# Performance work log

Hardware: AMD Instinct MI355X
Metric: run time of the kernel (lower is better)

The kernel has to match this reference:

```python
import jax, jax.numpy as jnp
import numpy as np

B, S, A, C, E, H = 256, 512, 8, 256, 64, 256

def _lin_params(key, din, dout):
    k1, k2 = jax.random.split(key)
    bound = 1.0 / np.sqrt(din)
    w = jax.random.uniform(k1, (din, dout), minval=-bound, maxval=bound, dtype=jnp.float32)
    b = jax.random.uniform(k2, (dout,), minval=-bound, maxval=bound, dtype=jnp.float32)
    return w, b

def setup_inputs() -> dict:
    key = jax.random.key(0)
    ks = jax.random.split(key, 9)
    q = jax.random.normal(ks[0], (B, S, A), dtype=jnp.float32)
    st = jax.random.normal(ks[1], (B, S, C), dtype=jnp.float32)
    w1a, b1a = _lin_params(ks[2], C, H)
    w1b, b1b = _lin_params(ks[3], H, A * E)
    w2a, b2a = _lin_params(ks[4], C, H)
    w2b, b2b = _lin_params(ks[5], H, E)
    wb1, bb1 = _lin_params(ks[6], C, E)
    wb2a, bb2a = _lin_params(ks[7], C, H)
    wb2b, bb2b = _lin_params(ks[8], H, 1)
    return dict(agent_q_values=q, central_states=st,
                w1a=w1a, b1a=b1a, w1b=w1b, b1b=b1b,
                w2a=w2a, b2a=b2a, w2b=w2b, b2b=b2b,
                wb1=wb1, bb1=bb1,
                wb2a=wb2a, bb2a=bb2a, wb2b=wb2b, bb2b=bb2b)

def _mlp(x, wa, ba, wb, bb):
    # Linear -> ELU -> Linear
    h = jax.nn.elu(x @ wa + ba)
    return h @ wb + bb

def reference(agent_q_values, central_states,
              w1a, b1a, w1b, b1b,
              w2a, b2a, w2b, b2b,
              wb1, bb1,
              wb2a, bb2a, wb2b, bb2b):
    bsz, seq, na = agent_q_values.shape
    st = central_states.reshape(-1, C)                      # [N, C]
    q = agent_q_values.reshape(-1, na)                      # [N, A]
    w1 = jnp.abs(_mlp(st, w1a, b1a, w1b, b1b)).reshape(-1, na, E)   # [N, A, E]
    b1 = st @ wb1 + bb1                                     # [N, E]
    w2 = jnp.abs(_mlp(st, w2a, b2a, w2b, b2b))              # [N, E]
    b2 = _mlp(st, wb2a, bb2a, wb2b, bb2b)                   # [N, 1]
    hidden = jax.nn.relu(jnp.einsum('na,nae->ne', q, w1) + b1)      # [N, E]
    joint = jnp.einsum('ne,ne->n', hidden, w2)[:, None] + b2        # [N, 1]
    return joint.reshape(bsz, seq, 1)
```

## Files before the change

kernel.cpp:

```cpp
#include <hip/hip_runtime.h>
#include <math.h>

typedef __bf16 bf16_t;
typedef bf16_t bf16x8 __attribute__((ext_vector_type(8)));
typedef float  floatx4 __attribute__((ext_vector_type(4)));

#define MFMA16(a, b, c) __builtin_amdgcn_mfma_f32_16x16x32_bf16((a), (b), (c), 0, 0, 0)

constexpr int NTOT = 256 * 512;
constexpr int CDIM = 256;

constexpr int N_TILES  = 88;
constexpr int WS_ELEMS = N_TILES * 4096;

__global__ void prep_weights(const float* __restrict__ w1a, const float* __restrict__ w1b,
                             const float* __restrict__ w2a, const float* __restrict__ w2b,
                             const float* __restrict__ wb1, const float* __restrict__ wb2a,
                             bf16_t* __restrict__ ws) {
  int idx = blockIdx.x * 256 + threadIdx.x;
  if (idx >= WS_ELEMS) return;
  int t   = idx >> 12;
  int rel = idx & 4095;
  const float* src; int dout; int ct;
  if      (t < 16) { src = w1a;  dout = 256; ct = t; }
  else if (t < 20) { src = wb1;  dout = 64;  ct = t - 16; }
  else if (t < 52) { src = w1b;  dout = 512; ct = t - 20; }
  else if (t < 68) { src = w2a;  dout = 256; ct = t - 52; }
  else if (t < 72) { src = w2b;  dout = 64;  ct = t - 68; }
  else             { src = wb2a; dout = 256; ct = t - 72; }
  int j    = rel & 7;
  int lane = (rel >> 3) & 63;
  int ks   = rel >> 9;
  int o = ct * 16 + (lane & 15);
  int k = ks * 32 + (lane >> 4) * 8 + j;
  ws[idx] = (bf16_t)src[(size_t)k * dout + o];
}

__device__ __forceinline__ void gload_lds16(const bf16_t* g, bf16_t* l) {
  __builtin_amdgcn_global_load_lds(
      (const __attribute__((address_space(1))) unsigned int*)g,
      (__attribute__((address_space(3))) unsigned int*)l, 16, 0, 0);
}

__global__ __launch_bounds__(256, 4)
void mixing_fused(const float* __restrict__ q,
                  const float* __restrict__ st,
                  const bf16_t* __restrict__ W,
                  const float* __restrict__ b1a, const float* __restrict__ b1b,
                  const float* __restrict__ b2a, const float* __restrict__ b2b,
                  const float* __restrict__ bb1,
                  const float* __restrict__ bb2a,
                  const float* __restrict__ wb2b, const float* __restrict__ bb2b,
                  float* __restrict__ out) {
  __shared__ __align__(16) bf16_t wbuf[2][8192];
  __shared__ __align__(16) bf16_t t_s[4][16][36];
  __shared__ __align__(16) float  q_s[4][128];

  const int tid  = threadIdx.x;
  const int wid  = tid >> 6;
  const int lane = tid & 63;
  const int l15  = lane & 15;
  const int quad = lane >> 4;
  const int m0   = blockIdx.x * 64 + wid * 16;

  auto stage = [&](int g) {
    const bf16_t* src = W + (size_t)g * 8192 + wid * 2048 + lane * 8;
    bf16_t* dst = &wbuf[g & 1][wid * 2048];
#pragma unroll
    for (int i = 0; i < 4; ++i)
      gload_lds16(src + i * 512, dst + i * 512);
  };

  *(float2*)&q_s[wid][lane * 2] = *(const float2*)(q + (size_t)m0 * 8 + lane * 2);

  bf16x8 sA[8];
  {
    const float* rp = st + (size_t)(m0 + l15) * CDIM;
#pragma unroll
    for (int ks = 0; ks < 8; ++ks) {
      int k0 = ks * 32 + quad * 8;
      float4 f0 = *(const float4*)(rp + k0);
      float4 f1 = *(const float4*)(rp + k0 + 4);
      bf16x8 v;
      v[0] = (bf16_t)f0.x; v[1] = (bf16_t)f0.y; v[2] = (bf16_t)f0.z; v[3] = (bf16_t)f0.w;
      v[4] = (bf16_t)f1.x; v[5] = (bf16_t)f1.y; v[6] = (bf16_t)f1.z; v[7] = (bf16_t)f1.w;
      sA[ks] = v;
    }
  }

  auto gemmL = [&](int buf, int h, const bf16x8 (&A)[8], floatx4& acc) {
    floatx4 z = {0.f, 0.f, 0.f, 0.f};
    acc = z;
#pragma unroll
    for (int kk = 0; kk < 8; ++kk) {
      bf16x8 b = *(const bf16x8*)&wbuf[buf][h * 4096 + kk * 512 + lane * 8];
      acc = MFMA16(A[kk], b, acc);
    }
  };

  stage(0);

  bf16x8 hA[8];

#pragma unroll
  for (int ks = 0; ks < 8; ++ks) {
    __syncthreads();
    stage(ks + 1);
    const int buf = ks & 1;
#pragma unroll
    for (int h = 0; h < 2; ++h) {
      int ct = 2 * ks + h;
      floatx4 acc;
      gemmL(buf, h, sA, acc);
      float bias = b1a[ct * 16 + l15];
#pragma unroll
      for (int i = 0; i < 4; ++i) {
        float v = acc[i] + bias;
        v = v > 0.f ? v : (__expf(v) - 1.f);
        t_s[wid][quad * 4 + i][h * 16 + l15] = (bf16_t)v;
      }
    }
    hA[ks] = *(const bf16x8*)&t_s[wid][l15][quad * 8];
  }

  floatx4 hid[4];
#pragma unroll
  for (int gg = 0; gg < 2; ++gg) {
    __syncthreads();
    stage(9 + gg);
    const int buf = gg & 1;
#pragma unroll
    for (int h = 0; h < 2; ++h) {
      int et = 2 * gg + h;
      floatx4 acc;
      gemmL(buf, h, sA, acc);
      float bias = bb1[et * 16 + l15];
      hid[et] = acc + bias;
    }
  }

#pragma unroll 1
  for (int a = 0; a < 8; ++a) {
    float qv[4];
#pragma unroll
    for (int i = 0; i < 4; ++i)
      qv[i] = q_s[wid][(quad * 4 + i) * 8 + a];
#pragma unroll
    for (int g2 = 0; g2 < 2; ++g2) {
      const int idx = a * 2 + g2;
      __syncthreads();
      stage(11 + idx);
      const int buf = g2;
#pragma unroll
      for (int h = 0; h < 2; ++h) {
        int ct = a * 4 + g2 * 2 + h;
        const int et = g2 * 2 + h;
        floatx4 acc;
        gemmL(buf, h, hA, acc);
        float bias = b1b[ct * 16 + l15];
#pragma unroll
        for (int i = 0; i < 4; ++i) {
          float w1v = fabsf(acc[i] + bias);
          hid[et][i] += qv[i] * w1v;
        }
      }
    }
  }
#pragma unroll
  for (int et = 0; et < 4; ++et)
#pragma unroll
    for (int i = 0; i < 4; ++i) hid[et][i] = fmaxf(hid[et][i], 0.f);

#pragma unroll
  for (int ks = 0; ks < 8; ++ks) {
    __syncthreads();
    stage(27 + ks);
    const int buf = ks & 1;
#pragma unroll
    for (int h = 0; h < 2; ++h) {
      int ct = 2 * ks + h;
      floatx4 acc;
      gemmL(buf, h, sA, acc);
      float bias = b2a[ct * 16 + l15];
#pragma unroll
      for (int i = 0; i < 4; ++i) {
        float v = acc[i] + bias;
        v = v > 0.f ? v : (__expf(v) - 1.f);
        t_s[wid][quad * 4 + i][h * 16 + l15] = (bf16_t)v;
      }
    }
    hA[ks] = *(const bf16x8*)&t_s[wid][l15][quad * 8];
  }

  float p[4] = {0.f, 0.f, 0.f, 0.f};
#pragma unroll
  for (int gg = 0; gg < 2; ++gg) {
    __syncthreads();
    stage(35 + gg);
    const int buf = gg & 1;
#pragma unroll
    for (int h = 0; h < 2; ++h) {
      int et = 2 * gg + h;
      floatx4 acc;
      gemmL(buf, h, hA, acc);
      float bias = b2b[et * 16 + l15];
#pragma unroll
      for (int i = 0; i < 4; ++i) {
        float w2v = fabsf(acc[i] + bias);
        p[i] += hid[et][i] * w2v;
      }
    }
  }

#pragma unroll 1
  for (int gg = 0; gg < 8; ++gg) {
    __syncthreads();
    if (gg < 7) stage(37 + gg);
    const int buf = gg & 1;
#pragma unroll
    for (int h = 0; h < 2; ++h) {
      int ct = 2 * gg + h;
      floatx4 acc;
      gemmL(buf, h, sA, acc);
      float bias = bb2a[ct * 16 + l15];
      float wv   = wb2b[ct * 16 + l15];
#pragma unroll
      for (int i = 0; i < 4; ++i) {
        float v = acc[i] + bias;
        v = v > 0.f ? v : (__expf(v) - 1.f);
        p[i] += v * wv;
      }
    }
  }

  float bb2 = bb2b[0];
#pragma unroll
  for (int i = 0; i < 4; ++i) {
    float v = p[i];
    v += __shfl_xor(v, 1);
    v += __shfl_xor(v, 2);
    v += __shfl_xor(v, 4);
    v += __shfl_xor(v, 8);
    if (l15 == 0) out[m0 + quad * 4 + i] = v + bb2;
  }
}

extern "C" void kernel_launch(void* const* d_in, const int* in_sizes, int n_in,
                              void* d_out, int out_size, void* d_ws, size_t ws_size,
                              hipStream_t stream) {
  const float* q    = (const float*)d_in[0];
  const float* st   = (const float*)d_in[1];
  const float* w1a  = (const float*)d_in[2];
  const float* b1a  = (const float*)d_in[3];
  const float* w1b  = (const float*)d_in[4];
  const float* b1b  = (const float*)d_in[5];
  const float* w2a  = (const float*)d_in[6];
  const float* b2a  = (const float*)d_in[7];
  const float* w2b  = (const float*)d_in[8];
  const float* b2b  = (const float*)d_in[9];
  const float* wb1  = (const float*)d_in[10];
  const float* bb1  = (const float*)d_in[11];
  const float* wb2a = (const float*)d_in[12];
  const float* bb2a = (const float*)d_in[13];
  const float* wb2b = (const float*)d_in[14];
  const float* bb2b = (const float*)d_in[15];
  bf16_t* W = (bf16_t*)d_ws;

  hipLaunchKernelGGL(prep_weights, dim3((WS_ELEMS + 255) / 256), dim3(256), 0, stream,
                     w1a, w1b, w2a, w2b, wb1, wb2a, W);
  hipLaunchKernelGGL(mixing_fused, dim3(NTOT / 64), dim3(256), 0, stream,
                     q, st, W, b1a, b1b, b2a, b2b, bb1, bb2a, wb2b, bb2b, (float*)d_out);
}
```

Baseline: 320.3 us.

## Split weight tiles between LDS staging and direct global-to-register loads

Each 8192-element weight group is now split in half: the first 4096-element column tile is still staged into LDS via global_load_lds, and the second tile is loaded straight from global memory into registers (Bd) for its MFMA sequence. This halves LDS usage and the LDS read traffic per group. The cost is higher register pressure, so launch bounds drop from 4 to 3 blocks per CU, and the direct global loads may sit on the critical path with latency that is not hidden.

```diff
diff --git a/kernel.cpp b/kernel.cpp
--- a/kernel.cpp
+++ b/kernel.cpp
@@ -42,7 +42,7 @@
       (__attribute__((address_space(3))) unsigned int*)l, 16, 0, 0);
 }
 
-__global__ __launch_bounds__(256, 4)
+__global__ __launch_bounds__(256, 3)
 void mixing_fused(const float* __restrict__ q,
                   const float* __restrict__ st,
                   const bf16_t* __restrict__ W,
@@ -52,7 +52,7 @@
                   const float* __restrict__ bb2a,
                   const float* __restrict__ wb2b, const float* __restrict__ bb2b,
                   float* __restrict__ out) {
-  __shared__ __align__(16) bf16_t wbuf[2][8192];
+  __shared__ __align__(16) bf16_t wbuf[2][4096];
   __shared__ __align__(16) bf16_t t_s[4][16][36];
   __shared__ __align__(16) float  q_s[4][128];
 
@@ -64,11 +64,19 @@
   const int m0   = blockIdx.x * 64 + wid * 16;
 
   auto stage = [&](int g) {
-    const bf16_t* src = W + (size_t)g * 8192 + wid * 2048 + lane * 8;
-    bf16_t* dst = &wbuf[g & 1][wid * 2048];
-#pragma unroll
-    for (int i = 0; i < 4; ++i)
+    const bf16_t* src = W + (size_t)g * 8192 + wid * 1024 + lane * 8;
+    bf16_t* dst = &wbuf[g & 1][wid * 1024];
+#pragma unroll
+    for (int i = 0; i < 2; ++i)
       gload_lds16(src + i * 512, dst + i * 512);
+  };
+
+  bf16x8 Bd[8];
+  auto LDd = [&](int g) {
+    const bf16_t* wp = W + (size_t)g * 8192 + 4096 + lane * 8;
+#pragma unroll
+    for (int kk = 0; kk < 8; ++kk)
+      Bd[kk] = *(const bf16x8*)(wp + kk * 512);
   };
 
   *(float2*)&q_s[wid][lane * 2] = *(const float2*)(q + (size_t)m0 * 8 + lane * 2);
@@ -88,15 +96,22 @@
     }
   }
 
-  auto gemmL = [&](int buf, int h, const bf16x8 (&A)[8], floatx4& acc) {
+  auto gemmS = [&](int buf, const bf16x8 (&A)[8], floatx4& acc) {
     floatx4 z = {0.f, 0.f, 0.f, 0.f};
     acc = z;
 #pragma unroll
     for (int kk = 0; kk < 8; ++kk) {
-      bf16x8 b = *(const bf16x8*)&wbuf[buf][h * 4096 + kk * 512 + lane * 8];
+      bf16x8 b = *(const bf16x8*)&wbuf[buf][kk * 512 + lane * 8];
       acc = MFMA16(A[kk], b, acc);
     }
   };
+  auto gemmR = [&](const bf16x8 (&A)[8], floatx4& acc) {
+    floatx4 z = {0.f, 0.f, 0.f, 0.f};
+    acc = z;
+#pragma unroll
+    for (int kk = 0; kk < 8; ++kk)
+      acc = MFMA16(A[kk], Bd[kk], acc);
+  };
 
   stage(0);
 
@@ -105,19 +120,29 @@
 #pragma unroll
   for (int ks = 0; ks < 8; ++ks) {
     __syncthreads();
+    LDd(ks);
     stage(ks + 1);
     const int buf = ks & 1;
-#pragma unroll
-    for (int h = 0; h < 2; ++h) {
-      int ct = 2 * ks + h;
-      floatx4 acc;
-      gemmL(buf, h, sA, acc);
-      float bias = b1a[ct * 16 + l15];
-#pragma unroll
-      for (int i = 0; i < 4; ++i) {
-        float v = acc[i] + bias;
-        v = v > 0.f ? v : (__expf(v) - 1.f);
-        t_s[wid][quad * 4 + i][h * 16 + l15] = (bf16_t)v;
+    {
+      floatx4 acc;
+      gemmS(buf, sA, acc);
+      float bias = b1a[(2 * ks) * 16 + l15];
+#pragma unroll
+      for (int i = 0; i < 4; ++i) {
+        float v = acc[i] + bias;
+        v = v > 0.f ? v : (__expf(v) - 1.f);
+        t_s[wid][quad * 4 + i][l15] = (bf16_t)v;
+      }
+    }
+    {
+      floatx4 acc;
+      gemmR(sA, acc);
+      float bias = b1a[(2 * ks + 1) * 16 + l15];
+#pragma unroll
+      for (int i = 0; i < 4; ++i) {
+        float v = acc[i] + bias;
+        v = v > 0.f ? v : (__expf(v) - 1.f);
+        t_s[wid][quad * 4 + i][16 + l15] = (bf16_t)v;
       }
     }
     hA[ks] = *(const bf16x8*)&t_s[wid][l15][quad * 8];
@@ -127,15 +152,18 @@
 #pragma unroll
   for (int gg = 0; gg < 2; ++gg) {
     __syncthreads();
+    LDd(8 + gg);
     stage(9 + gg);
     const int buf = gg & 1;
-#pragma unroll
-    for (int h = 0; h < 2; ++h) {
-      int et = 2 * gg + h;
-      floatx4 acc;
-      gemmL(buf, h, sA, acc);
-      float bias = bb1[et * 16 + l15];
-      hid[et] = acc + bias;
+    {
+      floatx4 acc;
+      gemmS(buf, sA, acc);
+      hid[2 * gg] = acc + bb1[(2 * gg) * 16 + l15];
+    }
+    {
+      floatx4 acc;
+      gemmR(sA, acc);
+      hid[2 * gg + 1] = acc + bb1[(2 * gg + 1) * 16 + l15];
     }
   }
 
@@ -149,21 +177,31 @@
     for (int g2 = 0; g2 < 2; ++g2) {
       const int idx = a * 2 + g2;
       __syncthreads();
+      LDd(10 + idx);
       stage(11 + idx);
       const int buf = g2;
-#pragma unroll
-      for (int h = 0; h < 2; ++h) {
-        int ct = a * 4 + g2 * 2 + h;
-        const int et = g2 * 2 + h;
+      {
+        const int et = g2 * 2;
         floatx4 acc;
-        gemmL(buf, h, hA, acc);
-        float bias = b1b[ct * 16 + l15];
+        gemmS(buf, hA, acc);
+        float bias = b1b[(a * 4 + g2 * 2) * 16 + l15];
 #pragma unroll
         for (int i = 0; i < 4; ++i) {
           float w1v = fabsf(acc[i] + bias);
           hid[et][i] += qv[i] * w1v;
         }
       }
+      {
+        const int et = g2 * 2 + 1;
+        floatx4 acc;
+        gemmR(hA, acc);
+        float bias = b1b[(a * 4 + g2 * 2 + 1) * 16 + l15];
+#pragma unroll
+        for (int i = 0; i < 4; ++i) {
+          float w1v = fabsf(acc[i] + bias);
+          hid[et][i] += qv[i] * w1v;
+        }
+      }
     }
   }
 #pragma unroll
@@ -174,19 +212,29 @@
 #pragma unroll
   for (int ks = 0; ks < 8; ++ks) {
     __syncthreads();
+    LDd(26 + ks);
     stage(27 + ks);
     const int buf = ks & 1;
-#pragma unroll
-    for (int h = 0; h < 2; ++h) {
-      int ct = 2 * ks + h;
-      floatx4 acc;
-      gemmL(buf, h, sA, acc);
-      float bias = b2a[ct * 16 + l15];
-#pragma unroll
-      for (int i = 0; i < 4; ++i) {
-        float v = acc[i] + bias;
-        v = v > 0.f ? v : (__expf(v) - 1.f);
-        t_s[wid][quad * 4 + i][h * 16 + l15] = (bf16_t)v;
+    {
+      floatx4 acc;
+      gemmS(buf, sA, acc);
+      float bias = b2a[(2 * ks) * 16 + l15];
+#pragma unroll
+      for (int i = 0; i < 4; ++i) {
+        float v = acc[i] + bias;
+        v = v > 0.f ? v : (__expf(v) - 1.f);
+        t_s[wid][quad * 4 + i][l15] = (bf16_t)v;
+      }
+    }
+    {
+      floatx4 acc;
+      gemmR(sA, acc);
+      float bias = b2a[(2 * ks + 1) * 16 + l15];
+#pragma unroll
+      for (int i = 0; i < 4; ++i) {
+        float v = acc[i] + bias;
+        v = v > 0.f ? v : (__expf(v) - 1.f);
+        t_s[wid][quad * 4 + i][16 + l15] = (bf16_t)v;
       }
     }
     hA[ks] = *(const bf16x8*)&t_s[wid][l15][quad * 8];
@@ -196,13 +244,13 @@
 #pragma unroll
   for (int gg = 0; gg < 2; ++gg) {
     __syncthreads();
+    LDd(34 + gg);
     stage(35 + gg);
     const int buf = gg & 1;
-#pragma unroll
-    for (int h = 0; h < 2; ++h) {
-      int et = 2 * gg + h;
-      floatx4 acc;
-      gemmL(buf, h, hA, acc);
+    {
+      const int et = 2 * gg;
+      floatx4 acc;
+      gemmS(buf, hA, acc);
       float bias = b2b[et * 16 + l15];
 #pragma unroll
       for (int i = 0; i < 4; ++i) {
@@ -210,18 +258,42 @@
         p[i] += hid[et][i] * w2v;
       }
     }
+    {
+      const int et = 2 * gg + 1;
+      floatx4 acc;
+      gemmR(hA, acc);
+      float bias = b2b[et * 16 + l15];
+#pragma unroll
+      for (int i = 0; i < 4; ++i) {
+        float w2v = fabsf(acc[i] + bias);
+        p[i] += hid[et][i] * w2v;
+      }
+    }
   }
 
 #pragma unroll 1
   for (int gg = 0; gg < 8; ++gg) {
     __syncthreads();
+    LDd(36 + gg);
     if (gg < 7) stage(37 + gg);
     const int buf = gg & 1;
-#pragma unroll
-    for (int h = 0; h < 2; ++h) {
-      int ct = 2 * gg + h;
-      floatx4 acc;
-      gemmL(buf, h, sA, acc);
+    {
+      int ct = 2 * gg;
+      floatx4 acc;
+      gemmS(buf, sA, acc);
+      float bias = bb2a[ct * 16 + l15];
+      float wv   = wb2b[ct * 16 + l15];
+#pragma unroll
+      for (int i = 0; i < 4; ++i) {
+        float v = acc[i] + bias;
+        v = v > 0.f ? v : (__expf(v) - 1.f);
+        p[i] += v * wv;
+      }
+    }
+    {
+      int ct = 2 * gg + 1;
+      floatx4 acc;
+      gemmR(sA, acc);
       float bias = bb2a[ct * 16 + l15];
       float wv   = wb2b[ct * 16 + l15];
 #pragma unroll
```

After: 354.1 us. 10.5% more time.
